# Kernel optimization log

Measured on AMD Instinct MI355X. Metric: run time of the kernel, lower is better.

The kernel has to match this reference:

```python
import jax, jax.numpy as jnp
import numpy as np

N, S, E, H = 2, 2048, 1024, 16
D = E // H  # head_dim = 64


def setup_inputs() -> dict:
    key = jax.random.key(0)
    k1, k2, k3 = jax.random.split(key, 3)
    x = jax.random.normal(k1, (N, S, E), dtype=jnp.float32)
    # Xavier-uniform-scaled weights (torch Linear layout: [out_features, in_features])
    lim_qkv = (6.0 / (E + 3 * E)) ** 0.5
    qkv_w = jax.random.uniform(k2, (3 * E, E), dtype=jnp.float32, minval=-lim_qkv, maxval=lim_qkv)
    lim_o = (6.0 / (E + E)) ** 0.5
    o_w = jax.random.uniform(k3, (E, E), dtype=jnp.float32, minval=-lim_o, maxval=lim_o)
    # causal look-ahead mask: positions where mask == 0 are excluded
    attn_mask = jnp.tril(jnp.ones((S, S), dtype=jnp.int32))
    return {"x": x, "attn_mask": attn_mask, "qkv_w": qkv_w, "o_w": o_w}


def reference(x, attn_mask, qkv_w, o_w):
    n, s, e = x.shape
    qkv = x @ qkv_w.T                              # (N, S, 3E)
    q, k, v = jnp.split(qkv, 3, axis=-1)
    # (N, S, E) -> (N, H, S, D)
    def to_heads(t):
        return t.reshape(n, s, H, D).transpose(0, 2, 1, 3)
    q, k, v = to_heads(q), to_heads(k), to_heads(v)
    scale = 1.0 / jnp.sqrt(jnp.asarray(D, dtype=x.dtype))
    logits = jnp.einsum('bhqd,bhkd->bhqk', q, k) * scale   # (N, H, S, S)
    mask = attn_mask.reshape(1, 1, s, s)                    # expand_mask: 2D -> (1,1,S,S)
    logits = jnp.where(mask == 0, -jnp.inf, logits)
    attn_weights = jax.nn.softmax(logits, axis=-1)
    values = jnp.einsum('bhqk,bhkd->bhqd', attn_weights, v)  # (N, H, S, D)
    values = values.transpose(0, 2, 1, 3).reshape(n, s, e)
    o = values @ o_w.T
    return o
```

## Files before the change

kernel.cpp:

```cpp
#include <hip/hip_runtime.h>
#include <math.h>

typedef unsigned short u16;
typedef unsigned int uint;
typedef __attribute__((ext_vector_type(8))) short bf16x8;
typedef __attribute__((ext_vector_type(4))) float floatx4;

__device__ __forceinline__ u16 f2bf(float f) {
  union { float f; uint u; } c; c.f = f;
  return (u16)((c.u + 0x7FFFu + ((c.u >> 16) & 1u)) >> 16);
}
__device__ __forceinline__ float bf2f(u16 h) {
  union { uint u; float f; } c; c.u = ((uint)h) << 16;
  return c.f;
}

#if __has_builtin(__builtin_amdgcn_exp2f)
#define EX2 __builtin_amdgcn_exp2f
#else
#define EX2 exp2f
#endif

__device__ __forceinline__ void gl_lds16(const u16* g, u16* l) {
  __builtin_amdgcn_global_load_lds(
      (const __attribute__((address_space(1))) uint*)g,
      (__attribute__((address_space(3))) uint*)l, 16, 0, 0);
}

__device__ __forceinline__ void store_c(u16* p, float v) { *p = f2bf(v); }
__device__ __forceinline__ void store_c(float* p, float v) { *p = v; }

#define ROR16(x, n)                                                        \
  __builtin_bit_cast(float, __builtin_amdgcn_update_dpp(                   \
      __builtin_bit_cast(int, (x)), __builtin_bit_cast(int, (x)),          \
      0x120 + (n), 0xF, 0xF, false))
__device__ __forceinline__ float rmax16(float x) {
  x = fmaxf(x, ROR16(x, 8)); x = fmaxf(x, ROR16(x, 4));
  x = fmaxf(x, ROR16(x, 2)); x = fmaxf(x, ROR16(x, 1));
  return x;
}
__device__ __forceinline__ float rsum16(float x) {
  x += ROR16(x, 8); x += ROR16(x, 4); x += ROR16(x, 2); x += ROR16(x, 1);
  return x;
}

__global__ __launch_bounds__(256) void cvt_all(const float* __restrict__ x,
                                               const float* __restrict__ qw,
                                               const float* __restrict__ ow,
                                               u16* __restrict__ xb,
                                               u16* __restrict__ wb,
                                               u16* __restrict__ ob) {
  int bx = blockIdx.x;
  const float* src; u16* dst; int off;
  if (bx < 2048) { src = x; dst = xb; off = bx; }
  else if (bx < 3584) { src = qw; dst = wb; off = bx - 2048; }
  else { src = ow; dst = ob; off = bx - 3584; }
  int i = (off * 256 + threadIdx.x) * 8;
  float4 a = *(const float4*)(src + i);
  float4 b = *(const float4*)(src + i + 4);
  bf16x8 r;
  r[0] = (short)f2bf(a.x); r[1] = (short)f2bf(a.y);
  r[2] = (short)f2bf(a.z); r[3] = (short)f2bf(a.w);
  r[4] = (short)f2bf(b.x); r[5] = (short)f2bf(b.y);
  r[6] = (short)f2bf(b.z); r[7] = (short)f2bf(b.w);
  *(bf16x8*)(dst + i) = r;
}

__global__ __launch_bounds__(256) void vtrans(const u16* __restrict__ qkv,
                                              u16* __restrict__ vt) {
  constexpr int S = 2048, E = 1024, TE = 3072;
  __shared__ u16 tile[64 * 72];
  const int t = threadIdx.x;
  const int kv0 = blockIdx.x * 64;
  const int bh = blockIdx.y, b = bh >> 4, h = bh & 15;
  const u16* src = qkv + (size_t)b * S * TE + 2 * E + h * 64;
#pragma unroll
  for (int i = 0; i < 2; ++i) {
    int c = t + i * 256;
    int kv = c >> 3, d0 = (c & 7) * 8;
    *(bf16x8*)&tile[kv * 72 + d0] = *(const bf16x8*)&src[(size_t)(kv0 + kv) * TE + d0];
  }
  __syncthreads();
  u16* dst = vt + (size_t)bh * 64 * S + kv0;
#pragma unroll
  for (int i = 0; i < 2; ++i) {
    int c = t + i * 256;
    int d = c >> 3, k0 = (c & 7) * 8;
    bf16x8 r;
#pragma unroll
    for (int j = 0; j < 8; ++j) r[j] = tile[(k0 + j) * 72 + d];
    *(bf16x8*)&dst[(size_t)d * S + k0] = r;
  }
}

template <typename TC>
__global__ __launch_bounds__(256) void gemm_bt(const u16* __restrict__ A,
                                               const u16* __restrict__ B,
                                               TC* __restrict__ C,
                                               int K, int N) {
  __shared__ __align__(16) u16 lds_a[128 * 64];
  __shared__ __align__(16) u16 lds_b[128 * 64];
  const int t = threadIdx.x;
  const int w = t >> 6, lane = t & 63, quad = lane >> 4, lr = lane & 15;
  const int wr = w >> 1, wc = w & 1;
  const int m0 = blockIdx.y * 128, n0 = blockIdx.x * 128;

  const int srow = lane >> 3;
  const int scol = ((lane & 7) ^ srow) * 8;
  const u16* Ab = A + (size_t)(m0 + w * 32 + srow) * K + scol;
  const u16* Bb = B + (size_t)(n0 + w * 32 + srow) * K + scol;
  u16* la = lds_a + (w * 32) * 64;
  u16* lb = lds_b + (w * 32) * 64;

  floatx4 acc[4][4];
#pragma unroll
  for (int i = 0; i < 4; ++i)
#pragma unroll
    for (int j = 0; j < 4; ++j) acc[i][j] = {0.f, 0.f, 0.f, 0.f};

  for (int k0 = 0; k0 < K; k0 += 64) {
#pragma unroll
    for (int j = 0; j < 4; ++j) {
      gl_lds16(Ab + (size_t)(j * 8) * K + k0, la + j * 8 * 64);
      gl_lds16(Bb + (size_t)(j * 8) * K + k0, lb + j * 8 * 64);
    }
    __syncthreads();
#pragma unroll
    for (int kk = 0; kk < 2; ++kk) {
      bf16x8 af[4], bfr[4];
#pragma unroll
      for (int mi = 0; mi < 4; ++mi)
        af[mi] = *(const bf16x8*)&lds_a[(wr * 64 + mi * 16 + lr) * 64 +
                                        (((kk * 4 + quad) ^ (lr & 7)) * 8)];
#pragma unroll
      for (int ni = 0; ni < 4; ++ni)
        bfr[ni] = *(const bf16x8*)&lds_b[(wc * 64 + ni * 16 + lr) * 64 +
                                         (((kk * 4 + quad) ^ (lr & 7)) * 8)];
#pragma unroll
      for (int mi = 0; mi < 4; ++mi)
#pragma unroll
        for (int ni = 0; ni < 4; ++ni)
          acc[mi][ni] = __builtin_amdgcn_mfma_f32_16x16x32_bf16(
              af[mi], bfr[ni], acc[mi][ni], 0, 0, 0);
    }
    __syncthreads();
  }
#pragma unroll
  for (int mi = 0; mi < 4; ++mi)
#pragma unroll
    for (int r = 0; r < 4; ++r) {
      int m = m0 + wr * 64 + mi * 16 + quad * 4 + r;
#pragma unroll
      for (int ni = 0; ni < 4; ++ni) {
        int n = n0 + wc * 64 + ni * 16 + lr;
        store_c(&C[(size_t)m * N + n], acc[mi][ni][r]);
      }
    }
}

__global__ __launch_bounds__(256) void attn_fwd(const u16* __restrict__ qkv,
                                                const u16* __restrict__ vt,
                                                u16* __restrict__ out) {
  constexpr int S = 2048, E = 1024, TE = 3072;
  constexpr float NEG = -1e30f;
  __shared__ __align__(16) u16 lds_k[2][128 * 64];
  __shared__ __align__(16) u16 lds_vt[2][64 * 128];
  __shared__ __align__(16) u16 lds_p[64 * 128];
  const int t = threadIdx.x;
  const int w = t >> 6, lane = t & 63, quad = lane >> 4, lr = lane & 15;
  const int lin = (int)blockIdx.x;
  const int xcd = lin & 7, j = lin >> 3;
  const int bh = xcd + 8 * (j & 3);
  const int bx = j >> 2;
  const int b = bh >> 4, h = bh & 15;
  const size_t base = (size_t)b * S * TE;
  const u16* kbase = qkv + base + E + h * 64;
  const u16* vtb = vt + (size_t)bh * 64 * S;

  const int srow = lane >> 3;
  const int scol = ((lane & 7) ^ srow) * 8;
  const int vrow = lane >> 4;

  for (int ph = 0; ph < 2; ++ph) {
    const int qt = ph ? (31 - bx) : bx;
    const int q0 = qt * 64;
    const int nkt = (qt + 2) >> 1;

    const float QS = 0.125f * 1.44269504f;
    bf16x8 qf[2];
#pragma unroll
    for (int kk = 0; kk < 2; ++kk) {
      bf16x8 q = *(const bf16x8*)&qkv[base + (size_t)(q0 + w * 16 + lr) * TE +
                                      h * 64 + kk * 32 + quad * 8];
#pragma unroll
      for (int jj = 0; jj < 8; ++jj) q[jj] = (short)f2bf(bf2f((u16)q[jj]) * QS);
      qf[kk] = q;
    }

    float mst[4], lst[4];
    floatx4 oacc[4];
#pragma unroll
    for (int r = 0; r < 4; ++r) { mst[r] = NEG; lst[r] = 0.f; }
#pragma unroll
    for (int di = 0; di < 4; ++di) oacc[di] = {0.f, 0.f, 0.f, 0.f};

    __syncthreads();

#pragma unroll
    for (int i = 0; i < 4; ++i) {
      int r0 = w * 8 + i * 32;
      gl_lds16(kbase + (size_t)(r0 + srow) * TE + scol, &lds_k[0][r0 * 64]);
    }
#pragma unroll
    for (int i = 0; i < 4; ++i) {
      int d0 = w * 4 + i * 16;
      int d = d0 + vrow;
      int cbg = ((lane & 15) ^ (d & 15)) * 8;
      gl_lds16(vtb + (size_t)d * S + cbg, &lds_vt[0][d0 * 128]);
    }

    for (int kt = 0; kt < nkt; ++kt) {
      const int bi = kt & 1;
      __syncthreads();
      if (kt + 1 < nkt) {
        const int bn = bi ^ 1;
#pragma unroll
        for (int i = 0; i < 4; ++i) {
          int r0 = w * 8 + i * 32;
          gl_lds16(kbase + (size_t)(128 * (kt + 1) + r0 + srow) * TE + scol,
                   &lds_k[bn][r0 * 64]);
        }
#pragma unroll
        for (int i = 0; i < 4; ++i) {
          int d0 = w * 4 + i * 16;
          int d = d0 + vrow;
          int cbg = ((lane & 15) ^ (d & 15)) * 8;
          gl_lds16(vtb + (size_t)d * S + 128 * (kt + 1) + cbg,
                   &lds_vt[bn][d0 * 128]);
        }
      }

      floatx4 st[8];
#pragma unroll
      for (int ni = 0; ni < 8; ++ni) st[ni] = {0.f, 0.f, 0.f, 0.f};
#pragma unroll
      for (int kk = 0; kk < 2; ++kk) {
        bf16x8 kb[8];
#pragma unroll
        for (int ni = 0; ni < 8; ++ni)
          kb[ni] = *(const bf16x8*)&lds_k[bi][(ni * 16 + lr) * 64 +
                                             (((kk * 4 + quad) ^ (lr & 7)) * 8)];
#pragma unroll
        for (int ni = 0; ni < 8; ++ni)
          st[ni] = __builtin_amdgcn_mfma_f32_16x16x32_bf16(qf[kk], kb[ni], st[ni], 0, 0, 0);
      }

      const bool diag = (kt == nkt - 1);
      const int doff = (qt & 1) ? 64 : 0;
#pragma unroll
      for (int r = 0; r < 4; ++r) {
        const int rl = w * 16 + quad * 4 + r;
        if (diag) {
          const int thr = rl + doff;
#pragma unroll
          for (int ni = 0; ni < 8; ++ni)
            if (ni * 16 + lr > thr) st[ni][r] = NEG;
        }
        float tmax = NEG;
#pragma unroll
        for (int ni = 0; ni < 8; ++ni) tmax = fmaxf(tmax, st[ni][r]);
        tmax = rmax16(tmax);
        float mnew = fmaxf(mst[r], tmax);
        float alpha = EX2(mst[r] - mnew);
        float rsum = 0.f;
        const int swr = rl & 15;
#pragma unroll
        for (int ni = 0; ni < 8; ++ni) {
          float pv = EX2(st[ni][r] - mnew);
          rsum += pv;
          int cb = (ni << 1) + (lr >> 3);
          lds_p[rl * 128 + (((cb ^ swr) << 3) + (lr & 7))] = f2bf(pv);
        }
        rsum = rsum16(rsum);
        lst[r] = lst[r] * alpha + rsum;
        mst[r] = mnew;
#pragma unroll
        for (int di = 0; di < 4; ++di) oacc[di][r] *= alpha;
      }

#pragma unroll
      for (int kk = 0; kk < 4; ++kk) {
        const int rl2 = w * 16 + lr;
        bf16x8 pf = *(const bf16x8*)&lds_p[rl2 * 128 + ((((kk << 2) + quad) ^ lr) << 3)];
        bf16x8 vb[4];
#pragma unroll
        for (int di = 0; di < 4; ++di)
          vb[di] = *(const bf16x8*)&lds_vt[bi][(di * 16 + lr) * 128 +
                                              ((((kk << 2) + quad) ^ lr) << 3)];
#pragma unroll
        for (int di = 0; di < 4; ++di)
          oacc[di] = __builtin_amdgcn_mfma_f32_16x16x32_bf16(pf, vb[di], oacc[di], 0, 0, 0);
      }
    }

#pragma unroll
    for (int r = 0; r < 4; ++r) {
      int sg = q0 + w * 16 + quad * 4 + r;
      float inv_l = 1.f / lst[r];
#pragma unroll
      for (int di = 0; di < 4; ++di)
        out[((size_t)(b * S + sg)) * E + h * 64 + di * 16 + lr] =
            f2bf(oacc[di][r] * inv_l);
    }
  }
}

extern "C" void kernel_launch(void* const* d_in, const int* in_sizes, int n_in,
                              void* d_out, int out_size, void* d_ws, size_t ws_size,
                              hipStream_t stream) {
  constexpr int NB = 2, S = 2048, E = 1024;
  constexpr int M = NB * S;
  const float* x = (const float*)d_in[0];
  const float* qkv_w = (const float*)d_in[2];
  const float* o_w = (const float*)d_in[3];
  float* out = (float*)d_out;

  u16* qkv = (u16*)d_ws;
  u16* vt = qkv + (size_t)M * 3 * E;
  u16* xb = vt + (size_t)32 * 64 * S;
  u16* attn_o = xb;
  u16* wb = xb + (size_t)M * E;
  u16* ob = wb + (size_t)3 * E * E;

  cvt_all<<<4096, 256, 0, stream>>>(x, qkv_w, o_w, xb, wb, ob);
  gemm_bt<u16><<<dim3(3 * E / 128, M / 128), 256, 0, stream>>>(xb, wb, qkv, E, 3 * E);
  vtrans<<<dim3(S / 64, NB * 16), 256, 0, stream>>>(qkv, vt);
  attn_fwd<<<512, 256, 0, stream>>>(qkv, vt, attn_o);
  gemm_bt<float><<<dim3(E / 128, M / 128), 256, 0, stream>>>(attn_o, ob, out, E, E);
}
```

Baseline: 200.4 us.

## Split attention KV tile across two wave groups with LDS merge of partial softmax

The attention kernel doubles the block to 512 threads: four wave pairs share the same query rows, and each pair processes half of every 128-key tile. Each wave keeps a private P buffer, and at the end the two halves' running max, sum and output accumulators are merged through LDS using log-sum-exp rescaling. The aim is more waves in flight to hide latency and less serial per-wave work per tile. In exchange it adds an extra merge step with two block barriers, and the larger blocks may lower how many blocks fit per CU.

```diff
diff --git a/kernel.cpp b/kernel.cpp
--- a/kernel.cpp
+++ b/kernel.cpp
@@ -158,16 +158,18 @@
     }
 }
 
-__global__ __launch_bounds__(256) void attn_fwd(const u16* __restrict__ qkv,
-                                                const u16* __restrict__ vt,
-                                                u16* __restrict__ out) {
+__global__ __launch_bounds__(512, 4) void attn_fwd(const u16* __restrict__ qkv,
+                                                   const u16* __restrict__ vt,
+                                                   u16* __restrict__ out) {
   constexpr int S = 2048, E = 1024, TE = 3072;
   constexpr float NEG = -1e30f;
   __shared__ __align__(16) u16 lds_k[2][128 * 64];
   __shared__ __align__(16) u16 lds_vt[2][64 * 128];
-  __shared__ __align__(16) u16 lds_p[64 * 128];
+  __shared__ __align__(16) u16 lds_p[8 * 16 * 64];
   const int t = threadIdx.x;
   const int w = t >> 6, lane = t & 63, quad = lane >> 4, lr = lane & 15;
+  const int qw = w & 3;
+  const int kh = w >> 2;
   const int lin = (int)blockIdx.x;
   const int xcd = lin & 7, j = lin >> 3;
   const int bh = xcd + 8 * (j & 3);
@@ -180,6 +182,7 @@
   const int srow = lane >> 3;
   const int scol = ((lane & 7) ^ srow) * 8;
   const int vrow = lane >> 4;
+  u16* const pbase = lds_p + w * 1024;
 
   for (int ph = 0; ph < 2; ++ph) {
     const int qt = ph ? (31 - bx) : bx;
@@ -190,7 +193,7 @@
     bf16x8 qf[2];
 #pragma unroll
     for (int kk = 0; kk < 2; ++kk) {
-      bf16x8 q = *(const bf16x8*)&qkv[base + (size_t)(q0 + w * 16 + lr) * TE +
+      bf16x8 q = *(const bf16x8*)&qkv[base + (size_t)(q0 + qw * 16 + lr) * TE +
                                       h * 64 + kk * 32 + quad * 8];
 #pragma unroll
       for (int jj = 0; jj < 8; ++jj) q[jj] = (short)f2bf(bf2f((u16)q[jj]) * QS);
@@ -207,13 +210,13 @@
     __syncthreads();
 
 #pragma unroll
-    for (int i = 0; i < 4; ++i) {
-      int r0 = w * 8 + i * 32;
+    for (int i = 0; i < 2; ++i) {
+      int r0 = w * 8 + i * 64;
       gl_lds16(kbase + (size_t)(r0 + srow) * TE + scol, &lds_k[0][r0 * 64]);
     }
 #pragma unroll
-    for (int i = 0; i < 4; ++i) {
-      int d0 = w * 4 + i * 16;
+    for (int i = 0; i < 2; ++i) {
+      int d0 = w * 4 + i * 32;
       int d = d0 + vrow;
       int cbg = ((lane & 15) ^ (d & 15)) * 8;
       gl_lds16(vtb + (size_t)d * S + cbg, &lds_vt[0][d0 * 128]);
@@ -225,14 +228,14 @@
       if (kt + 1 < nkt) {
         const int bn = bi ^ 1;
 #pragma unroll
-        for (int i = 0; i < 4; ++i) {
-          int r0 = w * 8 + i * 32;
+        for (int i = 0; i < 2; ++i) {
+          int r0 = w * 8 + i * 64;
           gl_lds16(kbase + (size_t)(128 * (kt + 1) + r0 + srow) * TE + scol,
                    &lds_k[bn][r0 * 64]);
         }
 #pragma unroll
-        for (int i = 0; i < 4; ++i) {
-          int d0 = w * 4 + i * 16;
+        for (int i = 0; i < 2; ++i) {
+          int d0 = w * 4 + i * 32;
           int d = d0 + vrow;
           int cbg = ((lane & 15) ^ (d & 15)) * 8;
           gl_lds16(vtb + (size_t)d * S + 128 * (kt + 1) + cbg,
@@ -240,18 +243,20 @@
         }
       }
 
-      floatx4 st[8];
-#pragma unroll
-      for (int ni = 0; ni < 8; ++ni) st[ni] = {0.f, 0.f, 0.f, 0.f};
+      floatx4 st[4];
+#pragma unroll
+      for (int ni = 0; ni < 4; ++ni) st[ni] = {0.f, 0.f, 0.f, 0.f};
 #pragma unroll
       for (int kk = 0; kk < 2; ++kk) {
-        bf16x8 kb[8];
-#pragma unroll
-        for (int ni = 0; ni < 8; ++ni)
-          kb[ni] = *(const bf16x8*)&lds_k[bi][(ni * 16 + lr) * 64 +
+        bf16x8 kb[4];
+#pragma unroll
+        for (int ni = 0; ni < 4; ++ni) {
+          int kr = kh * 64 + ni * 16 + lr;
+          kb[ni] = *(const bf16x8*)&lds_k[bi][kr * 64 +
                                              (((kk * 4 + quad) ^ (lr & 7)) * 8)];
-#pragma unroll
-        for (int ni = 0; ni < 8; ++ni)
+        }
+#pragma unroll
+        for (int ni = 0; ni < 4; ++ni)
           st[ni] = __builtin_amdgcn_mfma_f32_16x16x32_bf16(qf[kk], kb[ni], st[ni], 0, 0, 0);
       }
 
@@ -259,27 +264,25 @@
       const int doff = (qt & 1) ? 64 : 0;
 #pragma unroll
       for (int r = 0; r < 4; ++r) {
-        const int rl = w * 16 + quad * 4 + r;
+        const int rw = quad * 4 + r;
         if (diag) {
-          const int thr = rl + doff;
-#pragma unroll
-          for (int ni = 0; ni < 8; ++ni)
-            if (ni * 16 + lr > thr) st[ni][r] = NEG;
-        }
-        float tmax = NEG;
-#pragma unroll
-        for (int ni = 0; ni < 8; ++ni) tmax = fmaxf(tmax, st[ni][r]);
+          const int thr = qw * 16 + rw + doff;
+#pragma unroll
+          for (int ni = 0; ni < 4; ++ni)
+            if (kh * 64 + ni * 16 + lr > thr) st[ni][r] = NEG;
+        }
+        float tmax = fmaxf(fmaxf(st[0][r], st[1][r]), fmaxf(st[2][r], st[3][r]));
         tmax = rmax16(tmax);
         float mnew = fmaxf(mst[r], tmax);
         float alpha = EX2(mst[r] - mnew);
         float rsum = 0.f;
-        const int swr = rl & 15;
-#pragma unroll
-        for (int ni = 0; ni < 8; ++ni) {
+        const int sw = rw & 7;
+#pragma unroll
+        for (int ni = 0; ni < 4; ++ni) {
           float pv = EX2(st[ni][r] - mnew);
           rsum += pv;
           int cb = (ni << 1) + (lr >> 3);
-          lds_p[rl * 128 + (((cb ^ swr) << 3) + (lr & 7))] = f2bf(pv);
+          pbase[rw * 64 + (((cb ^ sw) << 3) + (lr & 7))] = f2bf(pv);
         }
         rsum = rsum16(rsum);
         lst[r] = lst[r] * alpha + rsum;
@@ -289,28 +292,49 @@
       }
 
 #pragma unroll
-      for (int kk = 0; kk < 4; ++kk) {
-        const int rl2 = w * 16 + lr;
-        bf16x8 pf = *(const bf16x8*)&lds_p[rl2 * 128 + ((((kk << 2) + quad) ^ lr) << 3)];
+      for (int kk = 0; kk < 2; ++kk) {
+        bf16x8 pf = *(const bf16x8*)&pbase[lr * 64 +
+                                           ((((kk * 4 + quad) ^ (lr & 7)) << 3))];
         bf16x8 vb[4];
 #pragma unroll
-        for (int di = 0; di < 4; ++di)
+        for (int di = 0; di < 4; ++di) {
+          int cb = kh * 8 + kk * 4 + quad;
           vb[di] = *(const bf16x8*)&lds_vt[bi][(di * 16 + lr) * 128 +
-                                              ((((kk << 2) + quad) ^ lr) << 3)];
+                                               ((cb ^ lr) << 3)];
+        }
 #pragma unroll
         for (int di = 0; di < 4; ++di)
           oacc[di] = __builtin_amdgcn_mfma_f32_16x16x32_bf16(pf, vb[di], oacc[di], 0, 0, 0);
       }
     }
 
-#pragma unroll
-    for (int r = 0; r < 4; ++r) {
-      int sg = q0 + w * 16 + quad * 4 + r;
-      float inv_l = 1.f / lst[r];
-#pragma unroll
-      for (int di = 0; di < 4; ++di)
-        out[((size_t)(b * S + sg)) * E + h * 64 + di * 16 + lr] =
-            f2bf(oacc[di][r] * inv_l);
+    float* Os = (float*)&lds_k[0][0];
+    float* mls = (float*)&lds_vt[0][0];
+    __syncthreads();
+    if (kh == 1) {
+#pragma unroll
+      for (int r = 0; r < 4; ++r) {
+        int row = qw * 16 + quad * 4 + r;
+        if (lr == 0) { mls[row * 2] = mst[r]; mls[row * 2 + 1] = lst[r]; }
+#pragma unroll
+        for (int di = 0; di < 4; ++di) Os[row * 64 + di * 16 + lr] = oacc[di][r];
+      }
+    }
+    __syncthreads();
+    if (kh == 0) {
+#pragma unroll
+      for (int r = 0; r < 4; ++r) {
+        int row = qw * 16 + quad * 4 + r;
+        float m1 = mls[row * 2], l1 = mls[row * 2 + 1];
+        float m = fmaxf(mst[r], m1);
+        float a0 = EX2(mst[r] - m), a1 = EX2(m1 - m);
+        float inv_l = 1.f / (a0 * lst[r] + a1 * l1);
+        int sg = q0 + row;
+#pragma unroll
+        for (int di = 0; di < 4; ++di)
+          out[((size_t)(b * S + sg)) * E + h * 64 + di * 16 + lr] =
+              f2bf((a0 * oacc[di][r] + a1 * Os[row * 64 + di * 16 + lr]) * inv_l);
+      }
     }
   }
 }
@@ -335,6 +359,6 @@
   cvt_all<<<4096, 256, 0, stream>>>(x, qkv_w, o_w, xb, wb, ob);
   gemm_bt<u16><<<dim3(3 * E / 128, M / 128), 256, 0, stream>>>(xb, wb, qkv, E, 3 * E);
   vtrans<<<dim3(S / 64, NB * 16), 256, 0, stream>>>(qkv, vt);
-  attn_fwd<<<512, 256, 0, stream>>>(qkv, vt, attn_o);
+  attn_fwd<<<512, 512, 0, stream>>>(qkv, vt, attn_o);
   gemm_bt<float><<<dim3(E / 128, M / 128), 256, 0, stream>>>(attn_o, ob, out, E, E);
 }
```

Result: slower. 207.8 us (+3.7%).
